# Optimization experiments

Measured on AMD Instinct MI355X. Metric: run time of the kernel, lower is better.

## Reference

```python
import jax, jax.numpy as jnp
import numpy as np

B, N, D, K = 128, 512, 512, 8

def setup_inputs() -> dict:
    key = jax.random.key(0)
    ks = jax.random.split(key, 6)
    coefficients = jax.random.normal(ks[0], (B, N, D), dtype=jnp.float32)
    H = D // 2
    s1 = 1.0 / np.sqrt(D)
    s2 = 1.0 / np.sqrt(H)
    W1 = jax.random.uniform(ks[1], (D, H), jnp.float32, -s1, s1)
    b1 = jax.random.uniform(ks[2], (H,), jnp.float32, -s1, s1)
    W2 = jax.random.uniform(ks[3], (H,), jnp.float32, -s2, s2)
    b2 = jax.random.uniform(ks[4], (), jnp.float32, -s2, s2)
    base_logits = jnp.zeros((N,), jnp.float32)  # nn.Parameter(torch.zeros(n_freqs))
    return {"coefficients": coefficients, "W1": W1, "b1": b1, "W2": W2, "b2": b2,
            "base_logits": base_logits}

def reference(coefficients, W1, b1, W2, b2, base_logits):
    # scorer: Linear(D, D//2) -> GELU(exact) -> Linear(D//2, 1), squeeze last dim
    h = jax.nn.gelu(jnp.einsum('bnd,dh->bnh', coefficients, W1) + b1, approximate=False)
    logits = jnp.einsum('bnh,h->bn', h, W2) + b2 + base_logits[None, :]  # (B, N)
    # inference path (self.training == False): plain softmax, no gumbel noise
    probs = jax.nn.softmax(logits, axis=-1)
    _, indices = jax.lax.top_k(probs, K)                      # (B, K) int32
    mask = jnp.zeros_like(probs).at[jnp.arange(B)[:, None], indices].set(1.0)
    selected = jnp.take_along_axis(coefficients, indices[:, :, None], axis=1)  # (B, K, D)
    importance = probs  # softmax(logits) again in torch; identical in eval mode
    return selected, mask, importance, indices
```

## Files before the change

kernel.cpp:

```cpp
#include <hip/hip_runtime.h>
#include <math.h>

#define B_DIM 128
#define N_DIM 512
#define D_DIM 512
#define H_DIM 256
#define K_SEL 8

typedef _Float16 half8 __attribute__((ext_vector_type(8)));
typedef float    f32x4 __attribute__((ext_vector_type(4)));

__device__ __forceinline__ void gload_lds16(const void* g, void* l) {
    __builtin_amdgcn_global_load_lds((const __attribute__((address_space(1))) void*)g,
                                     (__attribute__((address_space(3))) void*)l, 16, 0, 0);
}

__global__ __launch_bounds__(512) void prep_w1_kernel(
    const float* __restrict__ W1,
    _Float16* __restrict__ w1frag_h,
    _Float16* __restrict__ w1frag_l)
{
    const int b    = blockIdx.x;
    const int c4   = b >> 4;
    const int ks   = b & 15;
    const int lane = threadIdx.x >> 3;
    const int j    = threadIdx.x & 7;
    const int col  = c4 * 16 + (lane & 15);
    const int k    = ks * 32 + (lane >> 4) * 8 + j;
    float x = W1[(size_t)k * H_DIM + col];
    _Float16 h = (_Float16)x;
    float r = x - (float)h;
    size_t o = (size_t)b * 512 + lane * 8 + j;
    w1frag_h[o] = h;
    w1frag_l[o] = (_Float16)(r * 2048.0f);
}

__global__ __launch_bounds__(512, 1) void fused_scorer_wlds(
    const float* __restrict__ X,
    const _Float16* __restrict__ w1frag_h,
    const _Float16* __restrict__ w1frag_l,
    const float* __restrict__ b1,
    const float* __restrict__ W2,
    float* __restrict__ lp)
{
    __shared__ half8 Wh[4096], Wl[4096];

    const int tid  = threadIdx.x;
    const int lane = tid & 63;
    const int wave = tid >> 6;
    const int l15  = lane & 15;
    const int lg   = lane >> 4;
    const int quarter = blockIdx.x >> 8;
    const int wgq     = blockIdx.x & 255;
    const int tok0 = (wgq * 8 + wave) * 32;

    #pragma unroll
    for (int c = wave; c < 64; c += 8) {
        size_t so = ((size_t)(quarter * 64 + c)) * 512 + lane * 8;
        gload_lds16(w1frag_h + so, &Wh[c * 64 + lane]);
        gload_lds16(w1frag_l + so, &Wl[c * 64 + lane]);
    }

    f32x4 acc[4][2], acc2[4][2];
    #pragma unroll
    for (int m = 0; m < 4; ++m)
        #pragma unroll
        for (int tg = 0; tg < 2; ++tg) {
            acc[m][tg]  = (f32x4){0.f, 0.f, 0.f, 0.f};
            acc2[m][tg] = (f32x4){0.f, 0.f, 0.f, 0.f};
        }

    const float* xp0 = X + (size_t)(tok0 + l15) * D_DIM + lg * 8;
    const float* xp1 = xp0 + (size_t)16 * D_DIM;

    auto split8 = [&](float4 a, float4 b, half8& hh, half8& ll) {
        float e[8] = {a.x, a.y, a.z, a.w, b.x, b.y, b.z, b.w};
        #pragma unroll
        for (int j = 0; j < 8; ++j) {
            _Float16 h = (_Float16)e[j];
            float r = e[j] - (float)h;
            hh[j] = h;
            ll[j] = (_Float16)(r * 2048.0f);
        }
    };

    float4 xvA[2][2], xvB[2][2];
    xvA[0][0] = *reinterpret_cast<const float4*>(xp0);
    xvA[0][1] = *reinterpret_cast<const float4*>(xp0 + 4);
    xvA[1][0] = *reinterpret_cast<const float4*>(xp1);
    xvA[1][1] = *reinterpret_cast<const float4*>(xp1 + 4);
    xvB[0][0] = *reinterpret_cast<const float4*>(xp0 + 32);
    xvB[0][1] = *reinterpret_cast<const float4*>(xp0 + 36);
    xvB[1][0] = *reinterpret_cast<const float4*>(xp1 + 32);
    xvB[1][1] = *reinterpret_cast<const float4*>(xp1 + 36);

    __syncthreads();

    #pragma unroll 2
    for (int ks2 = 0; ks2 < 16; ks2 += 2) {
        {
            half8 bxh[2], bxl[2];
            split8(xvA[0][0], xvA[0][1], bxh[0], bxl[0]);
            split8(xvA[1][0], xvA[1][1], bxh[1], bxl[1]);
            if (ks2 + 2 < 16) {
                const int ko = (ks2 + 2) * 32;
                xvA[0][0] = *reinterpret_cast<const float4*>(xp0 + ko);
                xvA[0][1] = *reinterpret_cast<const float4*>(xp0 + ko + 4);
                xvA[1][0] = *reinterpret_cast<const float4*>(xp1 + ko);
                xvA[1][1] = *reinterpret_cast<const float4*>(xp1 + ko + 4);
            }
            #pragma unroll
            for (int m = 0; m < 4; ++m) {
                const int c = (m * 16 + ks2) * 64 + lane;
                half8 wh = Wh[c];
                half8 wl = Wl[c];
                #pragma unroll
                for (int tg = 0; tg < 2; ++tg) {
                    acc[m][tg]  = __builtin_amdgcn_mfma_f32_16x16x32_f16(wh, bxh[tg], acc[m][tg],  0, 0, 0);
                    acc2[m][tg] = __builtin_amdgcn_mfma_f32_16x16x32_f16(wh, bxl[tg], acc2[m][tg], 0, 0, 0);
                    acc2[m][tg] = __builtin_amdgcn_mfma_f32_16x16x32_f16(wl, bxh[tg], acc2[m][tg], 0, 0, 0);
                }
            }
        }
        {
            half8 bxh[2], bxl[2];
            split8(xvB[0][0], xvB[0][1], bxh[0], bxl[0]);
            split8(xvB[1][0], xvB[1][1], bxh[1], bxl[1]);
            if (ks2 + 3 < 16) {
                const int ko = (ks2 + 3) * 32;
                xvB[0][0] = *reinterpret_cast<const float4*>(xp0 + ko);
                xvB[0][1] = *reinterpret_cast<const float4*>(xp0 + ko + 4);
                xvB[1][0] = *reinterpret_cast<const float4*>(xp1 + ko);
                xvB[1][1] = *reinterpret_cast<const float4*>(xp1 + ko + 4);
            }
            #pragma unroll
            for (int m = 0; m < 4; ++m) {
                const int c = (m * 16 + ks2 + 1) * 64 + lane;
                half8 wh = Wh[c];
                half8 wl = Wl[c];
                #pragma unroll
                for (int tg = 0; tg < 2; ++tg) {
                    acc[m][tg]  = __builtin_amdgcn_mfma_f32_16x16x32_f16(wh, bxh[tg], acc[m][tg],  0, 0, 0);
                    acc2[m][tg] = __builtin_amdgcn_mfma_f32_16x16x32_f16(wh, bxl[tg], acc2[m][tg], 0, 0, 0);
                    acc2[m][tg] = __builtin_amdgcn_mfma_f32_16x16x32_f16(wl, bxh[tg], acc2[m][tg], 0, 0, 0);
                }
            }
        }
    }

    float part[2] = {0.f, 0.f};
    #pragma unroll
    for (int m = 0; m < 4; ++m) {
        const int col4 = quarter * 64 + m * 16 + lg * 4;
        float4 b1v = *reinterpret_cast<const float4*>(b1 + col4);
        float4 w2v = *reinterpret_cast<const float4*>(W2 + col4);
        float bb[4] = {b1v.x, b1v.y, b1v.z, b1v.w};
        float ww[4] = {w2v.x, w2v.y, w2v.z, w2v.w};
        #pragma unroll
        for (int tg = 0; tg < 2; ++tg)
            #pragma unroll
            for (int r = 0; r < 4; ++r) {
                float z = acc[m][tg][r] + acc2[m][tg][r] * (1.0f / 2048.0f) + bb[r];
                float g = 0.5f * z * (1.0f + erff(z * 0.70710678118654752440f));
                part[tg] = fmaf(g, ww[r], part[tg]);
            }
    }
    #pragma unroll
    for (int tg = 0; tg < 2; ++tg) {
        float v = part[tg];
        v += __shfl_xor(v, 16, 64);
        v += __shfl_xor(v, 32, 64);
        if (lane < 16)
            lp[(size_t)quarter * 65536 + tok0 + tg * 16 + lane] = v;
    }
}

__global__ __launch_bounds__(256) void softmax_topk_kernel(
    const float* __restrict__ lp,
    const float* __restrict__ b2p,
    const float* __restrict__ base_logits,
    float* __restrict__ out_mask,
    float* __restrict__ out_importance,
    float* __restrict__ out_indices)
{
    const int b = blockIdx.x;
    const int tid = threadIdx.x;
    __shared__ float probs[N_DIM];
    __shared__ float redf[4];
    __shared__ int   redi[4];
    __shared__ int   sel_idx[K_SEL];

    const float b2v = b2p[0];
    int i0g = b * N_DIM + tid;
    int i1g = i0g + 256;
    float l0 = (lp[i0g] + lp[65536 + i0g]) + (lp[131072 + i0g] + lp[196608 + i0g]);
    float l1 = (lp[i1g] + lp[65536 + i1g]) + (lp[131072 + i1g] + lp[196608 + i1g]);
    l0 += b2v + base_logits[tid];
    l1 += b2v + base_logits[tid + 256];

    float m = fmaxf(l0, l1);
    #pragma unroll
    for (int s = 32; s >= 1; s >>= 1) m = fmaxf(m, __shfl_xor(m, s, 64));
    if ((tid & 63) == 0) redf[tid >> 6] = m;
    __syncthreads();
    float gm = fmaxf(fmaxf(redf[0], redf[1]), fmaxf(redf[2], redf[3]));
    __syncthreads();

    float e0 = expf(l0 - gm), e1 = expf(l1 - gm);
    float ssum = e0 + e1;
    #pragma unroll
    for (int s = 32; s >= 1; s >>= 1) ssum += __shfl_xor(ssum, s, 64);
    if ((tid & 63) == 0) redf[tid >> 6] = ssum;
    __syncthreads();
    float denom = redf[0] + redf[1] + redf[2] + redf[3];
    float p0 = e0 / denom, p1 = e1 / denom;
    probs[tid] = p0;
    probs[tid + 256] = p1;
    out_importance[b * N_DIM + tid] = p0;
    out_importance[b * N_DIM + tid + 256] = p1;
    __syncthreads();

    for (int it = 0; it < K_SEL; ++it) {
        float v0 = probs[tid]; int i0 = tid;
        float v1 = probs[tid + 256];
        if (v1 > v0) { v0 = v1; i0 = tid + 256; }
        #pragma unroll
        for (int s = 32; s >= 1; s >>= 1) {
            float ov = __shfl_xor(v0, s, 64);
            int   oi = __shfl_xor(i0, s, 64);
            if (ov > v0 || (ov == v0 && oi < i0)) { v0 = ov; i0 = oi; }
        }
        if ((tid & 63) == 0) { redf[tid >> 6] = v0; redi[tid >> 6] = i0; }
        __syncthreads();
        if (tid == 0) {
            float bv = redf[0]; int bi = redi[0];
            for (int w = 1; w < 4; ++w)
                if (redf[w] > bv || (redf[w] == bv && redi[w] < bi)) { bv = redf[w]; bi = redi[w]; }
            sel_idx[it] = bi;
            probs[bi] = -1.0f;
        }
        __syncthreads();
    }

    float mk0 = 0.f, mk1 = 0.f;
    #pragma unroll
    for (int i = 0; i < K_SEL; ++i) {
        if (sel_idx[i] == tid)       mk0 = 1.f;
        if (sel_idx[i] == tid + 256) mk1 = 1.f;
    }
    out_mask[b * N_DIM + tid] = mk0;
    out_mask[b * N_DIM + tid + 256] = mk1;

    if (tid < K_SEL) out_indices[b * K_SEL + tid] = (float)sel_idx[tid];
}

__global__ __launch_bounds__(256) void gather_kernel(
    const float* __restrict__ X,
    const float* __restrict__ out_indices,
    float* __restrict__ out_selected)
{
    const int b = blockIdx.x;
    const int tid = threadIdx.x;
    __shared__ int sel[K_SEL];
    if (tid < K_SEL) sel[tid] = (int)out_indices[b * K_SEL + tid];
    __syncthreads();
    #pragma unroll
    for (int i = 0; i < 4; ++i) {
        int f = tid + 256 * i;
        int ki = f >> 7;
        int c4 = f & 127;
        float4 v = reinterpret_cast<const float4*>(
            X + ((size_t)b * N_DIM + sel[ki]) * D_DIM)[c4];
        reinterpret_cast<float4*>(
            out_selected + ((size_t)b * K_SEL + ki) * D_DIM)[c4] = v;
    }
}

extern "C" void kernel_launch(void* const* d_in, const int* in_sizes, int n_in,
                              void* d_out, int out_size, void* d_ws, size_t ws_size,
                              hipStream_t stream) {
    const float* X           = (const float*)d_in[0];
    const float* W1          = (const float*)d_in[1];
    const float* b1          = (const float*)d_in[2];
    const float* W2          = (const float*)d_in[3];
    const float* b2          = (const float*)d_in[4];
    const float* base_logits = (const float*)d_in[5];

    float* out            = (float*)d_out;
    float* out_selected   = out;
    float* out_mask       = out_selected + B_DIM * K_SEL * D_DIM;
    float* out_importance = out_mask + B_DIM * N_DIM;
    float* out_indices    = out_importance + B_DIM * N_DIM;

    float*    lp       = out_selected;
    _Float16* w1frag_h = (_Float16*)(out_selected + 262144);
    _Float16* w1frag_l = (_Float16*)(out_selected + 327680);

    hipLaunchKernelGGL(prep_w1_kernel, dim3(256), dim3(512), 0, stream,
                       W1, w1frag_h, w1frag_l);
    hipLaunchKernelGGL(fused_scorer_wlds, dim3(1024), dim3(512), 0, stream,
                       X, w1frag_h, w1frag_l, b1, W2, lp);
    hipLaunchKernelGGL(softmax_topk_kernel, dim3(B_DIM), dim3(256), 0, stream,
                       lp, b2, base_logits, out_mask, out_importance, out_indices);
    hipLaunchKernelGGL(gather_kernel, dim3(B_DIM), dim3(256), 0, stream,
                       X, out_indices, out_selected);
}
```

Measured before the change: 119.0 us.

## Pre-split X into fp16 hi/lo MFMA fragments in workspace before scoring

Adds a prep kernel that converts X once into fp16 high/low split fragments laid out in MFMA order in the workspace. The scorer then loads ready-made half8 fragments instead of converting fp32 X four times, once per quarter block. Block-id decoding is remapped so the four quarter blocks sharing the same tokens run close together, which should improve L2 reuse. The cost is an extra pass that writes and reads back 128 MB of fp16 data, and the path only runs when the workspace is large enough.

```diff
diff --git a/kernel.cpp b/kernel.cpp
--- a/kernel.cpp
+++ b/kernel.cpp
@@ -35,6 +35,141 @@
     w1frag_l[o] = (_Float16)(r * 2048.0f);
 }
 
+__global__ __launch_bounds__(512) void prep_x_kernel(
+    const float* __restrict__ X,
+    _Float16* __restrict__ xfrag_h,
+    _Float16* __restrict__ xfrag_l)
+{
+    const int rb   = blockIdx.x;
+    const int lane = threadIdx.x & 63;
+    const int ks8  = threadIdx.x >> 6;
+    const int row  = rb * 16 + (lane & 15);
+    const int lg   = lane >> 4;
+    #pragma unroll
+    for (int kk = 0; kk < 2; ++kk) {
+        int ks = ks8 + kk * 8;
+        const float* xp = X + (size_t)row * D_DIM + ks * 32 + lg * 8;
+        float4 a = *reinterpret_cast<const float4*>(xp);
+        float4 b = *reinterpret_cast<const float4*>(xp + 4);
+        float e[8] = {a.x, a.y, a.z, a.w, b.x, b.y, b.z, b.w};
+        half8 hh, ll;
+        #pragma unroll
+        for (int j = 0; j < 8; ++j) {
+            _Float16 h = (_Float16)e[j];
+            float r = e[j] - (float)h;
+            hh[j] = h;
+            ll[j] = (_Float16)(r * 2048.0f);
+        }
+        size_t o = ((size_t)rb * 16 + ks) * 512 + lane * 8;
+        *reinterpret_cast<half8*>(xfrag_h + o) = hh;
+        *reinterpret_cast<half8*>(xfrag_l + o) = ll;
+    }
+}
+
+__device__ __forceinline__ void decode_bid(int bid, int& q, int& g) {
+    q = (bid >> 3) & 3;
+    g = ((bid >> 5) << 3) | (bid & 7);
+}
+
+__global__ __launch_bounds__(512, 1) void fused_scorer_wx(
+    const _Float16* __restrict__ xfrag_h,
+    const _Float16* __restrict__ xfrag_l,
+    const _Float16* __restrict__ w1frag_h,
+    const _Float16* __restrict__ w1frag_l,
+    const float* __restrict__ b1,
+    const float* __restrict__ W2,
+    float* __restrict__ lp)
+{
+    __shared__ half8 Wh[4096], Wl[4096];
+
+    const int tid  = threadIdx.x;
+    const int lane = tid & 63;
+    const int wave = tid >> 6;
+    const int lg   = lane >> 4;
+    int q, g;
+    decode_bid(blockIdx.x, q, g);
+    const int tok0 = (g * 8 + wave) * 32;
+    const int rb0  = tok0 >> 4;
+
+    #pragma unroll
+    for (int c = wave; c < 64; c += 8) {
+        size_t so = ((size_t)(q * 64 + c)) * 512 + lane * 8;
+        gload_lds16(w1frag_h + so, &Wh[c * 64 + lane]);
+        gload_lds16(w1frag_l + so, &Wl[c * 64 + lane]);
+    }
+
+    f32x4 acc[4][2], acc2[4][2];
+    #pragma unroll
+    for (int m = 0; m < 4; ++m)
+        #pragma unroll
+        for (int tg = 0; tg < 2; ++tg) {
+            acc[m][tg]  = (f32x4){0.f, 0.f, 0.f, 0.f};
+            acc2[m][tg] = (f32x4){0.f, 0.f, 0.f, 0.f};
+        }
+
+    const _Float16* xh0 = xfrag_h + ((size_t)(rb0)     * 16) * 512 + lane * 8;
+    const _Float16* xl0 = xfrag_l + ((size_t)(rb0)     * 16) * 512 + lane * 8;
+    const _Float16* xh1 = xfrag_h + ((size_t)(rb0 + 1) * 16) * 512 + lane * 8;
+    const _Float16* xl1 = xfrag_l + ((size_t)(rb0 + 1) * 16) * 512 + lane * 8;
+
+    half8 cxh0 = *reinterpret_cast<const half8*>(xh0);
+    half8 cxl0 = *reinterpret_cast<const half8*>(xl0);
+    half8 cxh1 = *reinterpret_cast<const half8*>(xh1);
+    half8 cxl1 = *reinterpret_cast<const half8*>(xl1);
+
+    __syncthreads();
+
+    #pragma unroll
+    for (int ks = 0; ks < 16; ++ks) {
+        half8 bxh0 = cxh0, bxl0 = cxl0, bxh1 = cxh1, bxl1 = cxl1;
+        if (ks < 15) {
+            const int o = (ks + 1) * 512;
+            cxh0 = *reinterpret_cast<const half8*>(xh0 + o);
+            cxl0 = *reinterpret_cast<const half8*>(xl0 + o);
+            cxh1 = *reinterpret_cast<const half8*>(xh1 + o);
+            cxl1 = *reinterpret_cast<const half8*>(xl1 + o);
+        }
+        #pragma unroll
+        for (int m = 0; m < 4; ++m) {
+            const int c = (m * 16 + ks) * 64 + lane;
+            half8 wh = Wh[c];
+            half8 wl = Wl[c];
+            acc[m][0]  = __builtin_amdgcn_mfma_f32_16x16x32_f16(wh, bxh0, acc[m][0],  0, 0, 0);
+            acc2[m][0] = __builtin_amdgcn_mfma_f32_16x16x32_f16(wh, bxl0, acc2[m][0], 0, 0, 0);
+            acc2[m][0] = __builtin_amdgcn_mfma_f32_16x16x32_f16(wl, bxh0, acc2[m][0], 0, 0, 0);
+            acc[m][1]  = __builtin_amdgcn_mfma_f32_16x16x32_f16(wh, bxh1, acc[m][1],  0, 0, 0);
+            acc2[m][1] = __builtin_amdgcn_mfma_f32_16x16x32_f16(wh, bxl1, acc2[m][1], 0, 0, 0);
+            acc2[m][1] = __builtin_amdgcn_mfma_f32_16x16x32_f16(wl, bxh1, acc2[m][1], 0, 0, 0);
+        }
+    }
+
+    float part[2] = {0.f, 0.f};
+    #pragma unroll
+    for (int m = 0; m < 4; ++m) {
+        const int col4 = q * 64 + m * 16 + lg * 4;
+        float4 b1v = *reinterpret_cast<const float4*>(b1 + col4);
+        float4 w2v = *reinterpret_cast<const float4*>(W2 + col4);
+        float bb[4] = {b1v.x, b1v.y, b1v.z, b1v.w};
+        float ww[4] = {w2v.x, w2v.y, w2v.z, w2v.w};
+        #pragma unroll
+        for (int tg = 0; tg < 2; ++tg)
+            #pragma unroll
+            for (int r = 0; r < 4; ++r) {
+                float z = acc[m][tg][r] + acc2[m][tg][r] * (1.0f / 2048.0f) + bb[r];
+                float gl = 0.5f * z * (1.0f + erff(z * 0.70710678118654752440f));
+                part[tg] = fmaf(gl, ww[r], part[tg]);
+            }
+    }
+    #pragma unroll
+    for (int tg = 0; tg < 2; ++tg) {
+        float v = part[tg];
+        v += __shfl_xor(v, 16, 64);
+        v += __shfl_xor(v, 32, 64);
+        if (lane < 16)
+            lp[(size_t)q * 65536 + tok0 + tg * 16 + lane] = v;
+    }
+}
+
 __global__ __launch_bounds__(512, 1) void fused_scorer_wlds(
     const float* __restrict__ X,
     const _Float16* __restrict__ w1frag_h,
@@ -50,8 +185,8 @@
     const int wave = tid >> 6;
     const int l15  = lane & 15;
     const int lg   = lane >> 4;
-    const int quarter = blockIdx.x >> 8;
-    const int wgq     = blockIdx.x & 255;
+    int quarter, wgq;
+    decode_bid(blockIdx.x, quarter, wgq);
     const int tok0 = (wgq * 8 + wave) * 32;
 
     #pragma unroll
@@ -161,8 +296,8 @@
             #pragma unroll
             for (int r = 0; r < 4; ++r) {
                 float z = acc[m][tg][r] + acc2[m][tg][r] * (1.0f / 2048.0f) + bb[r];
-                float g = 0.5f * z * (1.0f + erff(z * 0.70710678118654752440f));
-                part[tg] = fmaf(g, ww[r], part[tg]);
+                float gl = 0.5f * z * (1.0f + erff(z * 0.70710678118654752440f));
+                part[tg] = fmaf(gl, ww[r], part[tg]);
             }
     }
     #pragma unroll
@@ -298,8 +433,22 @@
 
     hipLaunchKernelGGL(prep_w1_kernel, dim3(256), dim3(512), 0, stream,
                        W1, w1frag_h, w1frag_l);
-    hipLaunchKernelGGL(fused_scorer_wlds, dim3(1024), dim3(512), 0, stream,
-                       X, w1frag_h, w1frag_l, b1, W2, lp);
+
+    const size_t XFRAG_ELEMS = (size_t)65536 * 512;
+    const size_t WS_NEEDED   = XFRAG_ELEMS * 2 * sizeof(_Float16);
+
+    if (ws_size >= WS_NEEDED) {
+        _Float16* xfrag_h = (_Float16*)d_ws;
+        _Float16* xfrag_l = xfrag_h + XFRAG_ELEMS;
+        hipLaunchKernelGGL(prep_x_kernel, dim3(4096), dim3(512), 0, stream,
+                           X, xfrag_h, xfrag_l);
+        hipLaunchKernelGGL(fused_scorer_wx, dim3(1024), dim3(512), 0, stream,
+                           xfrag_h, xfrag_l, w1frag_h, w1frag_l, b1, W2, lp);
+    } else {
+        hipLaunchKernelGGL(fused_scorer_wlds, dim3(1024), dim3(512), 0, stream,
+                           X, w1frag_h, w1frag_l, b1, W2, lp);
+    }
+
     hipLaunchKernelGGL(softmax_topk_kernel, dim3(B_DIM), dim3(256), 0, stream,
                        lp, b2, base_logits, out_mask, out_importance, out_indices);
     hipLaunchKernelGGL(gather_kernel, dim3(B_DIM), dim3(256), 0, stream,
```

Result: slower. 130.1 us (+9.3%).
